# Optimization experiments

Measured on AMD Instinct MI355X. Metric: run time of the kernel, lower is better.

The kernel has to match this reference:

```python
import jax, jax.numpy as jnp
import numpy as np

D_MODEL = 96
N_HEAD = 3
HEAD_DIM = D_MODEL // N_HEAD  # 32
D_FF = 2048
WIDTH = 65
HALF_W = (WIDTH - 1) // 2  # 32
EPS = 1e-5


def layer_norm(x, g, b):
    mu = jnp.mean(x, axis=-1, keepdims=True)
    var = jnp.mean(jnp.square(x - mu), axis=-1, keepdims=True)
    return (x - mu) * jax.lax.rsqrt(var + EPS) * g + b


def setup_inputs() -> dict:
    key = jax.random.key(0)
    ks = jax.random.split(key, 8)
    B, T = 8, 2048
    s = 0.05
    return {
        "x": jax.random.normal(ks[0], (B, D_MODEL, T), dtype=jnp.float32),
        "w_qkv": jax.random.normal(ks[1], (3 * D_MODEL, D_MODEL), dtype=jnp.float32) * s,
        "b_qkv": jnp.zeros((3 * D_MODEL,), dtype=jnp.float32),
        "w_out": jax.random.normal(ks[2], (D_MODEL, D_MODEL), dtype=jnp.float32) * s,
        "b_out": jnp.zeros((D_MODEL,), dtype=jnp.float32),
        "ln1_g": jnp.ones((D_MODEL,), dtype=jnp.float32),
        "ln1_b": jnp.zeros((D_MODEL,), dtype=jnp.float32),
        "w_ff1": jax.random.normal(ks[3], (D_FF, D_MODEL), dtype=jnp.float32) * s,
        "b_ff1": jnp.zeros((D_FF,), dtype=jnp.float32),
        "w_ff2": jax.random.normal(ks[4], (D_MODEL, D_FF), dtype=jnp.float32) * s,
        "b_ff2": jnp.zeros((D_MODEL,), dtype=jnp.float32),
        "ln2_g": jnp.ones((D_MODEL,), dtype=jnp.float32),
        "ln2_b": jnp.zeros((D_MODEL,), dtype=jnp.float32),
        "lnf_g": jnp.ones((D_MODEL,), dtype=jnp.float32),
        "lnf_b": jnp.zeros((D_MODEL,), dtype=jnp.float32),
    }


def reference(x, w_qkv, b_qkv, w_out, b_out, ln1_g, ln1_b, w_ff1, b_ff1,
              w_ff2, b_ff2, ln2_g, ln2_b, lnf_g, lnf_b):
    # x: (B, C, T) -> (B, T, C)
    h = jnp.transpose(x, (0, 2, 1))
    B, T, C = h.shape

    # --- multi-head self-attention with banded mask ---
    qkv = h @ w_qkv.T + b_qkv                      # (B, T, 3C)
    q, k, v = jnp.split(qkv, 3, axis=-1)
    q = q.reshape(B, T, N_HEAD, HEAD_DIM)
    k = k.reshape(B, T, N_HEAD, HEAD_DIM)
    v = v.reshape(B, T, N_HEAD, HEAD_DIM)

    scale = 1.0 / jnp.sqrt(jnp.float32(HEAD_DIM))
    scores = jnp.einsum("bthd,bshd->bhts", q, k) * scale  # (B, H, T, T)

    idx = jnp.arange(T)
    band = jnp.abs(idx[:, None] - idx[None, :]) <= HALF_W  # |i-j| <= half width
    scores = jnp.where(band[None, None], scores, jnp.float32(-jnp.inf))

    attn = jax.nn.softmax(scores, axis=-1)
    ctx = jnp.einsum("bhts,bshd->bthd", attn, v).reshape(B, T, C)
    attn_out = ctx @ w_out.T + b_out

    # --- post-norm encoder layer (dropout inactive / eval mode) ---
    h = layer_norm(h + attn_out, ln1_g, ln1_b)
    ff = jax.nn.relu(h @ w_ff1.T + b_ff1) @ w_ff2.T + b_ff2
    h = layer_norm(h + ff, ln2_g, ln2_b)

    # extra layernorm applied when width is not None
    h = layer_norm(h, lnf_g, lnf_b)

    # (B, T, C) -> (B, C, T)
    return jnp.transpose(h, (0, 2, 1))
```

## Files before the change

kernel.cpp:

```cpp
#include <hip/hip_runtime.h>
#include <hip/hip_bf16.h>

#define B 8
#define T 2048
#define C 96
#define NH 3
#define HD 32
#define FFD 2048
#define HALF_W 32
#define BT (B*T)

typedef __hip_bfloat16 bf16;
typedef __attribute__((ext_vector_type(8))) short short8;
typedef __attribute__((ext_vector_type(4))) short short4v;
typedef __attribute__((ext_vector_type(16))) float floatx16;

__device__ __forceinline__ short f2bs(float v){
    __hip_bfloat16 h = __float2bfloat16(v);
    return *reinterpret_cast<short*>(&h);
}
__device__ __forceinline__ float bs2f(short s){
    unsigned u = ((unsigned)(unsigned short)s) << 16;
    return __uint_as_float(u);
}
__device__ __forceinline__ int imin(int a, int b){ return a < b ? a : b; }
__device__ __forceinline__ int imax(int a, int b){ return a > b ? a : b; }
__device__ __forceinline__ short8 ld_b64x2(const short* p){
    short4v a = *(const short4v*)p;
    short4v b = *(const short4v*)(p + 4);
    short8 v;
    v[0]=a[0]; v[1]=a[1]; v[2]=a[2]; v[3]=a[3];
    v[4]=b[0]; v[5]=b[1]; v[6]=b[2]; v[7]=b[3];
    return v;
}

__global__ void cvtw_kernel(const float* __restrict__ wq, const float* __restrict__ wo,
                            const float* __restrict__ w1, const float* __restrict__ w2,
                            bf16* __restrict__ dst){
    int i = blockIdx.x*256 + threadIdx.x;
    if(i < 27648){
        int e = i&7, lane = (i>>3)&63, r = i>>9;
        int ks = r%6, ot = r/6;
        int o = ot*32 + (lane&31);
        int k = ks*16 + (lane>>5)*8 + e;
        dst[i] = __float2bfloat16(wq[o*96 + k]);
    } else if(i < 36864){
        int j = i - 27648;
        int e = j&7, lane = (j>>3)&63, r = j>>9;
        int ks = r%6, ct = r/6;
        int c = ct*32 + (lane&31);
        int k = ks*16 + (lane>>5)*8 + e;
        dst[i] = __float2bfloat16(wo[c*96 + k]);
    } else if(i < 233472){
        int j = i - 36864;
        int e = j&7, lane = (j>>3)&63, r = j>>9;
        int ks = r%6; r /= 6;
        int w = r%4, jt = r/4;
        int row = jt*128 + w*32 + (lane&31);
        int k = ks*16 + (lane>>5)*8 + e;
        dst[i] = __float2bfloat16(w1[row*96 + k]);
    } else if(i < 430080){
        int j = i - 233472;
        int e = j&7, lane = (j>>3)&63, r = j>>9;
        int ct = r%3; r /= 3;
        int g = r%2; r /= 2;
        int w = r%4, jt = r/4;
        int c = ct*32 + (lane&31);
        int k = jt*128 + w*32 + g*16 + (lane>>5)*8 + e;
        dst[i] = __float2bfloat16(w2[c*FFD + k]);
    }
}

__global__ __launch_bounds__(256) void qkv_kernel(
    const float* __restrict__ x, const bf16* __restrict__ wqs,
    const float* __restrict__ bias, bf16* __restrict__ qswz,
    bf16* __restrict__ kswz, bf16* __restrict__ vbuf){
    __shared__ float xs[96*36];
    int b  = blockIdx.x >> 6;
    int tt = blockIdx.x & 63;
    int t0 = tt * 32;
    for(int e = threadIdx.x; e < 96*8; e += 256){
        int c = e >> 3, t4 = e & 7;
        *(float4*)(xs + c*36 + t4*4) =
            *(const float4*)(x + (size_t)b*C*T + (size_t)c*T + t0 + t4*4);
    }
    __syncthreads();
    const int w = threadIdx.x >> 6, lane = threadIdx.x & 63;
    const int lm = lane & 31, hq = lane >> 5;
    short8 bfr[6];
    #pragma unroll
    for(int ks = 0; ks < 6; ++ks){
        short8 v;
        #pragma unroll
        for(int i = 0; i < 8; ++i)
            v[i] = f2bs(xs[(ks*16 + hq*8 + i)*36 + lm]);
        bfr[ks] = v;
    }
    int nacc = (w == 0) ? 3 : 2;
    int ots[3] = {w, w+4, 8};
    floatx16 acc[3];
    #pragma unroll
    for(int i = 0; i < 3; ++i)
        #pragma unroll
        for(int r = 0; r < 16; ++r) acc[i][r] = 0.f;
    #pragma unroll
    for(int i = 0; i < 3; ++i){
        if(i < nacc){
            #pragma unroll
            for(int ks = 0; ks < 6; ++ks){
                short8 af = *(const short8*)((const short*)wqs
                              + (size_t)(ots[i]*6 + ks)*512 + lane*8);
                acc[i] = __builtin_amdgcn_mfma_f32_32x32x16_bf16(af, bfr[ks], acc[i], 0,0,0);
            }
        }
    }
    #pragma unroll
    for(int i = 0; i < 3; ++i){
        if(i < nacc){
            int ot = ots[i];
            int pkq[4][2];
            #pragma unroll
            for(int q = 0; q < 4; ++q){
                float4 bv = *(const float4*)(bias + ot*32 + 8*q + 4*hq);
                short4v t;
                t[0] = f2bs(acc[i][4*q+0] + bv.x);
                t[1] = f2bs(acc[i][4*q+1] + bv.y);
                t[2] = f2bs(acc[i][4*q+2] + bv.z);
                t[3] = f2bs(acc[i][4*q+3] + bv.w);
                int2 u = *(int2*)&t;
                pkq[q][0] = u.x; pkq[q][1] = u.y;
            }
            if(ot < 6){
                int type = ot/3, hh = ot%3;
                short* base = (short*)(type == 0 ? qswz : kswz)
                            + ((size_t)(b*NH + hh)*64 + tt)*1024 + lane*8;
                #pragma unroll
                for(int g = 0; g < 2; ++g){
                    int a0 = pkq[2*g][0],   a1 = pkq[2*g][1];
                    int b0 = pkq[2*g+1][0], b1v = pkq[2*g+1][1];
                    int ra0 = __shfl_xor(a0, 32),  ra1 = __shfl_xor(a1, 32);
                    int rb0 = __shfl_xor(b0, 32),  rb1 = __shfl_xor(b1v, 32);
                    int4 sfi;
                    sfi.x = hq ? rb0 : a0;
                    sfi.y = hq ? rb1 : a1;
                    sfi.z = hq ? b0  : ra0;
                    sfi.w = hq ? b1v : ra1;
                    *(int4*)(base + g*512) = sfi;
                }
            } else {
                int hh = ot - 6;
                short* rowp = (short*)vbuf + ((size_t)(b*NH + hh)*T + t0 + lm)*32;
                #pragma unroll
                for(int q = 0; q < 4; ++q){
                    int2 u; u.x = pkq[q][0]; u.y = pkq[q][1];
                    *(int2*)(rowp + 8*q + 4*hq) = u;
                }
            }
        }
    }
}

__global__ __launch_bounds__(192) void attn_op_kernel(
    const bf16* __restrict__ qswz, const bf16* __restrict__ kswz,
    const bf16* __restrict__ vbuf, const bf16* __restrict__ wos,
    const float* __restrict__ bias, const float* __restrict__ x,
    const float* __restrict__ g1, const float* __restrict__ bb1,
    bf16* __restrict__ h1b){
    __shared__ __align__(16) short VtS[3*3200];
    __shared__ __align__(16) short PtS[3][3200];
    __shared__ float LsS[3][32];
    __shared__ __align__(16) short ctxS[32*100];
    __shared__ float red1[2][3][32];
    const int tid = threadIdx.x;
    const int w = tid / 64, lane = tid & 63;
    const int lm = lane & 31, hq = lane >> 5;
    int b  = blockIdx.x >> 6;
    int tt = blockIdx.x & 63;
    int t0 = tt * 32;

    short8 wof[6];
    #pragma unroll
    for(int ks = 0; ks < 6; ++ks)
        wof[ks] = *(const short8*)((const short*)wos + (size_t)(w*6 + ks)*512 + lane*8);

    for(int e = tid; e < 576; e += 192){
        int hh = e / 192, rem = e % 192;
        int kp = rem >> 2, d8 = rem & 3;
        const short* vb = (const short*)vbuf + (size_t)(b*NH + hh)*T*32;
        int sa = imin(imax(t0 - 32 + 2*kp, 0), T-1);
        int sb = imin(imax(t0 - 32 + 2*kp + 1, 0), T-1);
        short8 va = *(const short8*)(vb + (size_t)sa*32 + d8*8);
        short8 v2 = *(const short8*)(vb + (size_t)sb*32 + d8*8);
        #pragma unroll
        for(int j = 0; j < 8; ++j){
            int val = (int)(unsigned short)va[j] | ((int)(unsigned short)v2[j] << 16);
            *(int*)(VtS + hh*3200 + (d8*8 + j)*100 + 2*kp) = val;
        }
    }
    const short* qsw = (const short*)qswz + ((size_t)(b*NH + w)*64 + tt)*1024 + lane*8;
    short8 qf0 = *(const short8*)(qsw);
    short8 qf1 = *(const short8*)(qsw + 512);
    floatx16 S[3];
    #pragma unroll
    for(int sub = 0; sub < 3; ++sub){
        int kt = imin(imax(tt - 1 + sub, 0), 63);
        const short* ksw = (const short*)kswz + ((size_t)(b*NH + w)*64 + kt)*1024 + lane*8;
        short8 kf0 = *(const short8*)(ksw);
        short8 kf1 = *(const short8*)(ksw + 512);
        floatx16 z;
        #pragma unroll
        for(int r = 0; r < 16; ++r) z[r] = 0.f;
        z = __builtin_amdgcn_mfma_f32_32x32x16_bf16(kf0, qf0, z, 0,0,0);
        z = __builtin_amdgcn_mfma_f32_32x32x16_bf16(kf1, qf1, z, 0,0,0);
        S[sub] = z;
    }
    const float scale = 0.17677669529663687f;
    float part = 0.f;
    #pragma unroll
    for(int sub = 0; sub < 3; ++sub){
        #pragma unroll
        for(int r = 0; r < 16; ++r){
            int key_local = sub*32 + (r&3) + 8*(r>>2) + 4*hq;
            int s_glob = t0 - 32 + key_local;
            int rel = key_local - lm;
            bool ok = (rel >= 0) && (rel <= 64) && (s_glob >= 0) && (s_glob < T);
            float p = ok ? __expf(S[sub][r]*scale) : 0.f;
            S[sub][r] = p;
            part += p;
        }
    }
    float ltot = part + __shfl_xor(part, 32);
    if(hq == 0) LsS[w][lm] = ltot;
    #pragma unroll
    for(int sub = 0; sub < 3; ++sub){
        #pragma unroll
        for(int q4 = 0; q4 < 4; ++q4){
            int kbase = sub*32 + 8*q4 + 4*hq;
            short4v pk;
            pk[0] = f2bs(S[sub][4*q4+0]);
            pk[1] = f2bs(S[sub][4*q4+1]);
            pk[2] = f2bs(S[sub][4*q4+2]);
            pk[3] = f2bs(S[sub][4*q4+3]);
            *(short4v*)(PtS[w] + lm*100 + kbase) = pk;
        }
    }
    __syncthreads();
    floatx16 O;
    #pragma unroll
    for(int r = 0; r < 16; ++r) O[r] = 0.f;
    #pragma unroll
    for(int ks = 0; ks < 6; ++ks){
        short8 pa = ld_b64x2(PtS[w] + lm*100 + ks*16 + hq*8);
        short8 vf = ld_b64x2(VtS + w*3200 + lm*100 + ks*16 + hq*8);
        O = __builtin_amdgcn_mfma_f32_32x32x16_bf16(pa, vf, O, 0,0,0);
    }
    #pragma unroll
    for(int r = 0; r < 16; ++r){
        int qr = (r&3) + 8*(r>>2) + 4*hq;
        float linv = 1.f / LsS[w][qr];
        ctxS[qr*100 + w*32 + lm] = f2bs(O[r]*linv);
    }
    __syncthreads();

    short8 bfr[6];
    #pragma unroll
    for(int ks = 0; ks < 6; ++ks)
        bfr[ks] = ld_b64x2(ctxS + lm*100 + ks*16 + hq*8);
    floatx16 acc;
    #pragma unroll
    for(int r = 0; r < 16; ++r) acc[r] = 0.f;
    #pragma unroll
    for(int ks = 0; ks < 6; ++ks)
        acc = __builtin_amdgcn_mfma_f32_32x32x16_bf16(wof[ks], bfr[ks], acc, 0,0,0);
    float vals[16];
    float p1 = 0.f, p2 = 0.f;
    #pragma unroll
    for(int q = 0; q < 4; ++q){
        int c = w*32 + 8*q + 4*hq;
        float4 bv = *(const float4*)(bias + c);
        float bva[4] = {bv.x, bv.y, bv.z, bv.w};
        #pragma unroll
        for(int r = 0; r < 4; ++r){
            float xv = x[(size_t)b*C*T + (size_t)(c + r)*T + t0 + lm];
            float v = acc[4*q+r] + bva[r] + xv;
            vals[4*q+r] = v;
            p1 += v; p2 += v*v;
        }
    }
    p1 += __shfl_xor(p1, 32);
    p2 += __shfl_xor(p2, 32);
    if(hq == 0){ red1[0][w][lm] = p1; red1[1][w][lm] = p2; }
    __syncthreads();
    float s  = red1[0][0][lm] + red1[0][1][lm] + red1[0][2][lm];
    float s2 = red1[1][0][lm] + red1[1][1][lm] + red1[1][2][lm];
    float mu = s * (1.0f/96.0f);
    float rstd = rsqrtf(s2*(1.0f/96.0f) - mu*mu + 1e-5f);
    int row = b*T + t0 + lm;
    #pragma unroll
    for(int q = 0; q < 4; ++q){
        int c = w*32 + 8*q + 4*hq;
        float4 gv = *(const float4*)(g1 + c);
        float4 bv = *(const float4*)(bb1 + c);
        float ga[4] = {gv.x, gv.y, gv.z, gv.w};
        float ba[4] = {bv.x, bv.y, bv.z, bv.w};
        short4v pk;
        #pragma unroll
        for(int r = 0; r < 4; ++r)
            pk[r] = f2bs((vals[4*q+r] - mu)*rstd*ga[r] + ba[r]);
        *(short4v*)((short*)h1b + (size_t)row*96 + c) = pk;
    }
}

__global__ __launch_bounds__(256, 1) void ff_ln_kernel(
    const bf16* __restrict__ h1b,
    const bf16* __restrict__ w1s, const float* __restrict__ b1,
    const bf16* __restrict__ w2s, const float* __restrict__ b2,
    const float* __restrict__ g2, const float* __restrict__ bt2,
    const float* __restrict__ gf, const float* __restrict__ btf,
    float* __restrict__ out){
    __shared__ float redp[4*2*3*1088];
    __shared__ float zt[96*65];
    const int tid = threadIdx.x;
    const int w4 = tid >> 6, lane = tid & 63;
    const int lm = lane & 31, hq = lane >> 5;
    const int r0 = blockIdx.x * 64;
    short8 hf[2][6];
    #pragma unroll
    for(int mt = 0; mt < 2; ++mt)
        #pragma unroll
        for(int ks = 0; ks < 6; ++ks)
            hf[mt][ks] = *(const short8*)((const short*)h1b
                       + (size_t)(r0 + mt*32 + lm)*96 + ks*16 + hq*8);
    floatx16 acc2[2][3];
    #pragma unroll
    for(int mt = 0; mt < 2; ++mt)
        #pragma unroll
        for(int i = 0; i < 3; ++i)
            #pragma unroll
            for(int r = 0; r < 16; ++r) acc2[mt][i][r] = 0.f;

    const short* w1p = (const short*)w1s + (size_t)w4*6*512 + lane*8;
    const short* w2p = (const short*)w2s + (size_t)w4*2*3*512 + lane*8;
    short8 cw1[6], cw2[6];
    #pragma unroll
    for(int ks = 0; ks < 6; ++ks)
        cw1[ks] = *(const short8*)(w1p + ks*512);
    #pragma unroll
    for(int g = 0; g < 2; ++g)
        #pragma unroll
        for(int ct = 0; ct < 3; ++ct)
            cw2[g*3 + ct] = *(const short8*)(w2p + ((size_t)g*3 + ct)*512);

    #pragma unroll
    for(int jt = 0; jt < 16; ++jt){
        const int jn = (jt + 1) & 15;
        short8 nw1[6], nw2[6];
        #pragma unroll
        for(int ks = 0; ks < 6; ++ks)
            nw1[ks] = *(const short8*)(w1p + (size_t)jn*4*6*512 + ks*512);
        #pragma unroll
        for(int g = 0; g < 2; ++g)
            #pragma unroll
            for(int ct = 0; ct < 3; ++ct)
                nw2[g*3 + ct] = *(const short8*)(w2p + ((size_t)jn*4*2*3 + g*3 + ct)*512);
        floatx16 a0, a1;
        #pragma unroll
        for(int r = 0; r < 16; ++r){ a0[r] = 0.f; a1[r] = 0.f; }
        #pragma unroll
        for(int ks = 0; ks < 6; ++ks){
            a0 = __builtin_amdgcn_mfma_f32_32x32x16_bf16(cw1[ks], hf[0][ks], a0, 0,0,0);
            a1 = __builtin_amdgcn_mfma_f32_32x32x16_bf16(cw1[ks], hf[1][ks], a1, 0,0,0);
        }
        int pk[2][4][2];
        #pragma unroll
        for(int q = 0; q < 4; ++q){
            float4 bv = *(const float4*)(b1 + jt*128 + w4*32 + 8*q + 4*hq);
            float bva[4] = {bv.x, bv.y, bv.z, bv.w};
            short4v t0v, t1v;
            #pragma unroll
            for(int r = 0; r < 4; ++r){
                float v0 = a0[4*q+r] + bva[r];
                float v1 = a1[4*q+r] + bva[r];
                t0v[r] = f2bs(v0 > 0.f ? v0 : 0.f);
                t1v[r] = f2bs(v1 > 0.f ? v1 : 0.f);
            }
            int2 u0 = *(int2*)&t0v; int2 u1 = *(int2*)&t1v;
            pk[0][q][0] = u0.x; pk[0][q][1] = u0.y;
            pk[1][q][0] = u1.x; pk[1][q][1] = u1.y;
        }
        #pragma unroll
        for(int g = 0; g < 2; ++g){
            short8 sf[2];
            #pragma unroll
            for(int mt = 0; mt < 2; ++mt){
                int a0i = pk[mt][2*g][0],   a1i = pk[mt][2*g][1];
                int b0i = pk[mt][2*g+1][0], b1i = pk[mt][2*g+1][1];
                int ra0 = __shfl_xor(a0i, 32), ra1 = __shfl_xor(a1i, 32);
                int rb0 = __shfl_xor(b0i, 32), rb1 = __shfl_xor(b1i, 32);
                int4 sfi;
                sfi.x = hq ? rb0 : a0i;
                sfi.y = hq ? rb1 : a1i;
                sfi.z = hq ? b0i : ra0;
                sfi.w = hq ? b1i : ra1;
                sf[mt] = *(short8*)&sfi;
            }
            #pragma unroll
            for(int ct = 0; ct < 3; ++ct){
                acc2[0][ct] = __builtin_amdgcn_mfma_f32_32x32x16_bf16(cw2[g*3+ct], sf[0], acc2[0][ct], 0,0,0);
                acc2[1][ct] = __builtin_amdgcn_mfma_f32_32x32x16_bf16(cw2[g*3+ct], sf[1], acc2[1][ct], 0,0,0);
            }
        }
        #pragma unroll
        for(int ks = 0; ks < 6; ++ks) cw1[ks] = nw1[ks];
        #pragma unroll
        for(int i = 0; i < 6; ++i) cw2[i] = nw2[i];
    }
    __syncthreads();
    #pragma unroll
    for(int mt = 0; mt < 2; ++mt)
        #pragma unroll
        for(int ct = 0; ct < 3; ++ct)
            #pragma unroll
            for(int q = 0; q < 4; ++q)
                #pragma unroll
                for(int r = 0; r < 4; ++r)
                    redp[((w4*2 + mt)*3 + ct)*1088 + lane*17 + 4*q + r] = acc2[mt][ct][4*q+r];
    __syncthreads();
    if(w4 < 2){
        const int mt = w4;
        const int rr = r0 + mt*32;
        float vals[48];
        float p1 = 0.f, p2 = 0.f;
        #pragma unroll
        for(int ct = 0; ct < 3; ++ct){
            #pragma unroll
            for(int q = 0; q < 4; ++q){
                int c = ct*32 + 8*q + 4*hq;
                float4 bv = *(const float4*)(b2 + c);
                short4v hv = *(const short4v*)((const short*)h1b + (size_t)(rr + lm)*96 + c);
                float bva[4] = {bv.x, bv.y, bv.z, bv.w};
                #pragma unroll
                for(int r = 0; r < 4; ++r){
                    float v = redp[((0*2 + mt)*3 + ct)*1088 + lane*17 + 4*q + r]
                            + redp[((1*2 + mt)*3 + ct)*1088 + lane*17 + 4*q + r]
                            + redp[((2*2 + mt)*3 + ct)*1088 + lane*17 + 4*q + r]
                            + redp[((3*2 + mt)*3 + ct)*1088 + lane*17 + 4*q + r]
                            + bva[r] + bs2f(hv[r]);
                    vals[ct*16 + 4*q + r] = v;
                    p1 += v; p2 += v*v;
                }
            }
        }
        p1 += __shfl_xor(p1, 32);
        p2 += __shfl_xor(p2, 32);
        float mu = p1*(1.0f/96.0f);
        float rstd = rsqrtf(p2*(1.0f/96.0f) - mu*mu + 1e-5f);
        float q1 = 0.f, q2 = 0.f;
        #pragma unroll
        for(int ct = 0; ct < 3; ++ct){
            #pragma unroll
            for(int q = 0; q < 4; ++q){
                int c = ct*32 + 8*q + 4*hq;
                float4 gv = *(const float4*)(g2 + c);
                float4 bv = *(const float4*)(bt2 + c);
                float ga[4] = {gv.x, gv.y, gv.z, gv.w};
                float ba[4] = {bv.x, bv.y, bv.z, bv.w};
                #pragma unroll
                for(int r = 0; r < 4; ++r){
                    float y = (vals[ct*16+4*q+r] - mu)*rstd*ga[r] + ba[r];
                    vals[ct*16+4*q+r] = y;
                    q1 += y; q2 += y*y;
                }
            }
        }
        q1 += __shfl_xor(q1, 32);
        q2 += __shfl_xor(q2, 32);
        float mu2 = q1*(1.0f/96.0f);
        float rstd2 = rsqrtf(q2*(1.0f/96.0f) - mu2*mu2 + 1e-5f);
        #pragma unroll
        for(int ct = 0; ct < 3; ++ct){
            #pragma unroll
            for(int q = 0; q < 4; ++q){
                int c = ct*32 + 8*q + 4*hq;
                float4 gv = *(const float4*)(gf + c);
                float4 bv = *(const float4*)(btf + c);
                float ga[4] = {gv.x, gv.y, gv.z, gv.w};
                float ba[4] = {bv.x, bv.y, bv.z, bv.w};
                #pragma unroll
                for(int r = 0; r < 4; ++r)
                    zt[(c + r)*65 + mt*32 + lm] = (vals[ct*16+4*q+r] - mu2)*rstd2*ga[r] + ba[r];
            }
        }
    }
    __syncthreads();
    int bb  = r0 / T;
    int t0g = r0 % T;
    for(int e = tid; e < 96*64; e += 256){
        int c = e >> 6, tt = e & 63;
        out[(size_t)bb*C*T + (size_t)c*T + t0g + tt] = zt[c*65 + tt];
    }
}

extern "C" void kernel_launch(void* const* d_in, const int* in_sizes, int n_in,
                              void* d_out, int out_size, void* d_ws, size_t ws_size,
                              hipStream_t stream) {
    const float* x     = (const float*)d_in[0];
    const float* w_qkv = (const float*)d_in[1];
    const float* b_qkv = (const float*)d_in[2];
    const float* w_out = (const float*)d_in[3];
    const float* b_out = (const float*)d_in[4];
    const float* ln1_g = (const float*)d_in[5];
    const float* ln1_b = (const float*)d_in[6];
    const float* w_ff1 = (const float*)d_in[7];
    const float* b_ff1 = (const float*)d_in[8];
    const float* w_ff2 = (const float*)d_in[9];
    const float* b_ff2 = (const float*)d_in[10];
    const float* ln2_g = (const float*)d_in[11];
    const float* ln2_b = (const float*)d_in[12];
    const float* lnf_g = (const float*)d_in[13];
    const float* lnf_b = (const float*)d_in[14];
    float* out = (float*)d_out;

    char* wsb = (char*)d_ws;
    bf16*  qswz  = (bf16*)wsb;
    bf16*  kswz  = (bf16*)(wsb + 3145728);
    bf16*  vbuf  = (bf16*)(wsb + 6291456);
    bf16*  h1b   = (bf16*)(wsb + 9437184);
    bf16*  wts   = (bf16*)(wsb + 12582912);
    bf16*  wqs   = wts;
    bf16*  wos   = wts + 27648;
    bf16*  w1s   = wts + 36864;
    bf16*  w2s   = wts + 233472;

    cvtw_kernel   <<<1680, 256, 0, stream>>>(w_qkv, w_out, w_ff1, w_ff2, wts);
    qkv_kernel    <<<BT/32, 256, 0, stream>>>(x, wqs, b_qkv, qswz, kswz, vbuf);
    attn_op_kernel<<<B*(T/32), 192, 0, stream>>>(qswz, kswz, vbuf, wos, b_out, x,
                                                 ln1_g, ln1_b, h1b);
    ff_ln_kernel  <<<BT/64, 256, 0, stream>>>(h1b, w1s, b_ff1, w2s, b_ff2,
                                              ln2_g, ln2_b, lnf_g, lnf_b, out);
}
```

Baseline: 126.6 us.

## Fuse QKV, banded attention, out-proj and FFN into one encoder kernel

Merges the QKV projection, attention with output projection and LN1, and the FFN with both layernorms into a single kernel. Each block handles 32 tokens and recomputes K and V for a 96-token halo instead of reading them back from global memory. This removes the q/k/v and h1 intermediate round-trips through global memory and two kernel launches. In exchange it repeats the K/V projection work about three times and runs the FFN with 32-row tiles and 192 threads instead of 64-row tiles, which means less weight reuse per block.

```diff
diff --git a/kernel.cpp b/kernel.cpp
--- a/kernel.cpp
+++ b/kernel.cpp
@@ -23,8 +23,6 @@
     unsigned u = ((unsigned)(unsigned short)s) << 16;
     return __uint_as_float(u);
 }
-__device__ __forceinline__ int imin(int a, int b){ return a < b ? a : b; }
-__device__ __forceinline__ int imax(int a, int b){ return a > b ? a : b; }
 __device__ __forceinline__ short8 ld_b64x2(const short* p){
     short4v a = *(const short4v*)p;
     short4v b = *(const short4v*)(p + 4);
@@ -32,6 +30,31 @@
     v[0]=a[0]; v[1]=a[1]; v[2]=a[2]; v[3]=a[3];
     v[4]=b[0]; v[5]=b[1]; v[6]=b[2]; v[7]=b[3];
     return v;
+}
+__device__ __forceinline__ int4 exch_pair(int a0,int a1,int b0,int b1,int hq){
+    int ra0=__shfl_xor(a0,32), ra1=__shfl_xor(a1,32);
+    int rb0=__shfl_xor(b0,32), rb1=__shfl_xor(b1,32);
+    int4 s;
+    s.x = hq ? rb0 : a0;
+    s.y = hq ? rb1 : a1;
+    s.z = hq ? b0  : ra0;
+    s.w = hq ? b1  : ra1;
+    return s;
+}
+__device__ __forceinline__ void proj_pack(const floatx16& acc, const float* bias32, int hq,
+                                          short8& f0, short8& f1){
+    int pkq[4][2];
+    #pragma unroll
+    for(int q = 0; q < 4; ++q){
+        float4 bv = *(const float4*)(bias32 + 8*q + 4*hq);
+        short4v t;
+        t[0]=f2bs(acc[4*q+0]+bv.x); t[1]=f2bs(acc[4*q+1]+bv.y);
+        t[2]=f2bs(acc[4*q+2]+bv.z); t[3]=f2bs(acc[4*q+3]+bv.w);
+        int2 u = *(int2*)&t; pkq[q][0]=u.x; pkq[q][1]=u.y;
+    }
+    int4 r0 = exch_pair(pkq[0][0],pkq[0][1],pkq[1][0],pkq[1][1],hq);
+    int4 r1 = exch_pair(pkq[2][0],pkq[2][1],pkq[3][0],pkq[3][1],hq);
+    f0 = *(short8*)&r0; f1 = *(short8*)&r1;
 }
 
 __global__ void cvtw_kernel(const float* __restrict__ wq, const float* __restrict__ wo,
@@ -71,147 +94,115 @@
     }
 }
 
-__global__ __launch_bounds__(256) void qkv_kernel(
-    const float* __restrict__ x, const bf16* __restrict__ wqs,
-    const float* __restrict__ bias, bf16* __restrict__ qswz,
-    bf16* __restrict__ kswz, bf16* __restrict__ vbuf){
-    __shared__ float xs[96*36];
-    int b  = blockIdx.x >> 6;
-    int tt = blockIdx.x & 63;
-    int t0 = tt * 32;
-    for(int e = threadIdx.x; e < 96*8; e += 256){
-        int c = e >> 3, t4 = e & 7;
-        *(float4*)(xs + c*36 + t4*4) =
-            *(const float4*)(x + (size_t)b*C*T + (size_t)c*T + t0 + t4*4);
-    }
-    __syncthreads();
-    const int w = threadIdx.x >> 6, lane = threadIdx.x & 63;
-    const int lm = lane & 31, hq = lane >> 5;
-    short8 bfr[6];
-    #pragma unroll
-    for(int ks = 0; ks < 6; ++ks){
-        short8 v;
-        #pragma unroll
-        for(int i = 0; i < 8; ++i)
-            v[i] = f2bs(xs[(ks*16 + hq*8 + i)*36 + lm]);
-        bfr[ks] = v;
-    }
-    int nacc = (w == 0) ? 3 : 2;
-    int ots[3] = {w, w+4, 8};
-    floatx16 acc[3];
-    #pragma unroll
-    for(int i = 0; i < 3; ++i)
-        #pragma unroll
-        for(int r = 0; r < 16; ++r) acc[i][r] = 0.f;
-    #pragma unroll
-    for(int i = 0; i < 3; ++i){
-        if(i < nacc){
-            #pragma unroll
-            for(int ks = 0; ks < 6; ++ks){
-                short8 af = *(const short8*)((const short*)wqs
-                              + (size_t)(ots[i]*6 + ks)*512 + lane*8);
-                acc[i] = __builtin_amdgcn_mfma_f32_32x32x16_bf16(af, bfr[ks], acc[i], 0,0,0);
-            }
-        }
-    }
-    #pragma unroll
-    for(int i = 0; i < 3; ++i){
-        if(i < nacc){
-            int ot = ots[i];
-            int pkq[4][2];
-            #pragma unroll
-            for(int q = 0; q < 4; ++q){
-                float4 bv = *(const float4*)(bias + ot*32 + 8*q + 4*hq);
-                short4v t;
-                t[0] = f2bs(acc[i][4*q+0] + bv.x);
-                t[1] = f2bs(acc[i][4*q+1] + bv.y);
-                t[2] = f2bs(acc[i][4*q+2] + bv.z);
-                t[3] = f2bs(acc[i][4*q+3] + bv.w);
-                int2 u = *(int2*)&t;
-                pkq[q][0] = u.x; pkq[q][1] = u.y;
-            }
-            if(ot < 6){
-                int type = ot/3, hh = ot%3;
-                short* base = (short*)(type == 0 ? qswz : kswz)
-                            + ((size_t)(b*NH + hh)*64 + tt)*1024 + lane*8;
-                #pragma unroll
-                for(int g = 0; g < 2; ++g){
-                    int a0 = pkq[2*g][0],   a1 = pkq[2*g][1];
-                    int b0 = pkq[2*g+1][0], b1v = pkq[2*g+1][1];
-                    int ra0 = __shfl_xor(a0, 32),  ra1 = __shfl_xor(a1, 32);
-                    int rb0 = __shfl_xor(b0, 32),  rb1 = __shfl_xor(b1v, 32);
-                    int4 sfi;
-                    sfi.x = hq ? rb0 : a0;
-                    sfi.y = hq ? rb1 : a1;
-                    sfi.z = hq ? b0  : ra0;
-                    sfi.w = hq ? b1v : ra1;
-                    *(int4*)(base + g*512) = sfi;
-                }
-            } else {
-                int hh = ot - 6;
-                short* rowp = (short*)vbuf + ((size_t)(b*NH + hh)*T + t0 + lm)*32;
-                #pragma unroll
-                for(int q = 0; q < 4; ++q){
-                    int2 u; u.x = pkq[q][0]; u.y = pkq[q][1];
-                    *(int2*)(rowp + 8*q + 4*hq) = u;
-                }
-            }
-        }
-    }
-}
-
-__global__ __launch_bounds__(192) void attn_op_kernel(
-    const bf16* __restrict__ qswz, const bf16* __restrict__ kswz,
-    const bf16* __restrict__ vbuf, const bf16* __restrict__ wos,
-    const float* __restrict__ bias, const float* __restrict__ x,
+__global__ __launch_bounds__(192, 2) void encoder_kernel(
+    const float* __restrict__ x,
+    const bf16* __restrict__ wqs, const bf16* __restrict__ wos,
+    const bf16* __restrict__ w1s, const bf16* __restrict__ w2s,
+    const float* __restrict__ b_qkv, const float* __restrict__ b_out,
     const float* __restrict__ g1, const float* __restrict__ bb1,
-    bf16* __restrict__ h1b){
-    __shared__ __align__(16) short VtS[3*3200];
-    __shared__ __align__(16) short PtS[3][3200];
-    __shared__ float LsS[3][32];
-    __shared__ __align__(16) short ctxS[32*100];
-    __shared__ float red1[2][3][32];
+    const float* __restrict__ b1, const float* __restrict__ b2,
+    const float* __restrict__ g2, const float* __restrict__ bt2,
+    const float* __restrict__ gf, const float* __restrict__ btf,
+    float* __restrict__ out){
+    __shared__ __align__(16) char smem[73088];
+    float* XS   = (float*)smem;
+    short* PTS  = (short*)smem;
+    float* REDP = (float*)smem;
+    short* VTS  = (short*)(smem + 39936);
+    float* ZT   = (float*)(smem + 39936);
+    short* CTX  = (short*)(smem + 59136);
+    short* H1S  = (short*)(smem + 65536);
+    float* LSS  = (float*)(smem + 71936);
+    float* RED1 = (float*)(smem + 72320);
+
     const int tid = threadIdx.x;
     const int w = tid / 64, lane = tid & 63;
     const int lm = lane & 31, hq = lane >> 5;
-    int b  = blockIdx.x >> 6;
-    int tt = blockIdx.x & 63;
-    int t0 = tt * 32;
+    const int b  = blockIdx.x >> 6;
+    const int tt = blockIdx.x & 63;
+    const int t0 = tt * 32;
+    const float* xb = x + (size_t)b*C*T;
 
     short8 wof[6];
     #pragma unroll
     for(int ks = 0; ks < 6; ++ks)
         wof[ks] = *(const short8*)((const short*)wos + (size_t)(w*6 + ks)*512 + lane*8);
 
-    for(int e = tid; e < 576; e += 192){
-        int hh = e / 192, rem = e % 192;
-        int kp = rem >> 2, d8 = rem & 3;
-        const short* vb = (const short*)vbuf + (size_t)(b*NH + hh)*T*32;
-        int sa = imin(imax(t0 - 32 + 2*kp, 0), T-1);
-        int sb = imin(imax(t0 - 32 + 2*kp + 1, 0), T-1);
-        short8 va = *(const short8*)(vb + (size_t)sa*32 + d8*8);
-        short8 v2 = *(const short8*)(vb + (size_t)sb*32 + d8*8);
-        #pragma unroll
-        for(int j = 0; j < 8; ++j){
-            int val = (int)(unsigned short)va[j] | ((int)(unsigned short)v2[j] << 16);
-            *(int*)(VtS + hh*3200 + (d8*8 + j)*100 + 2*kp) = val;
-        }
-    }
-    const short* qsw = (const short*)qswz + ((size_t)(b*NH + w)*64 + tt)*1024 + lane*8;
-    short8 qf0 = *(const short8*)(qsw);
-    short8 qf1 = *(const short8*)(qsw + 512);
+    int tg0 = t0 - 32;
+    if(tg0 >= 0 && t0 + 64 <= T){
+        for(int e = tid; e < 96*24; e += 192){
+            int c = e / 24, q4 = e % 24;
+            *(float4*)(XS + c*104 + q4*4) = *(const float4*)(xb + (size_t)c*T + tg0 + q4*4);
+        }
+    } else {
+        for(int e = tid; e < 96*96; e += 192){
+            int c = e / 96, j = e % 96;
+            int t = tg0 + j; t = t < 0 ? 0 : (t > T-1 ? T-1 : t);
+            XS[c*104 + j] = xb[(size_t)c*T + t];
+        }
+    }
+    __syncthreads();
+
+    short8 kwf[6], vwf[6];
+    #pragma unroll
+    for(int ks = 0; ks < 6; ++ks){
+        kwf[ks] = *(const short8*)((const short*)wqs + (size_t)((3+w)*6 + ks)*512 + lane*8);
+        vwf[ks] = *(const short8*)((const short*)wqs + (size_t)((6+w)*6 + ks)*512 + lane*8);
+    }
+    short8 kf[3][2]; short8 qf0, qf1;
+    #pragma unroll
+    for(int tau = 0; tau < 3; ++tau){
+        short8 bfr[6];
+        #pragma unroll
+        for(int ks = 0; ks < 6; ++ks){
+            short8 vv;
+            #pragma unroll
+            for(int i = 0; i < 8; ++i)
+                vv[i] = f2bs(XS[(ks*16 + hq*8 + i)*104 + tau*32 + lm]);
+            bfr[ks] = vv;
+        }
+        floatx16 acc;
+        #pragma unroll
+        for(int r = 0; r < 16; ++r) acc[r] = 0.f;
+        #pragma unroll
+        for(int ks = 0; ks < 6; ++ks)
+            acc = __builtin_amdgcn_mfma_f32_32x32x16_bf16(kwf[ks], bfr[ks], acc, 0,0,0);
+        proj_pack(acc, b_qkv + (3+w)*32, hq, kf[tau][0], kf[tau][1]);
+        #pragma unroll
+        for(int r = 0; r < 16; ++r) acc[r] = 0.f;
+        #pragma unroll
+        for(int ks = 0; ks < 6; ++ks)
+            acc = __builtin_amdgcn_mfma_f32_32x32x16_bf16(vwf[ks], bfr[ks], acc, 0,0,0);
+        #pragma unroll
+        for(int q = 0; q < 4; ++q){
+            float4 bv = *(const float4*)(b_qkv + (6+w)*32 + 8*q + 4*hq);
+            float bva[4] = {bv.x, bv.y, bv.z, bv.w};
+            #pragma unroll
+            for(int r = 0; r < 4; ++r)
+                VTS[w*3200 + (8*q + 4*hq + r)*100 + tau*32 + lm] = f2bs(acc[4*q+r] + bva[r]);
+        }
+        if(tau == 1){
+            floatx16 qa;
+            #pragma unroll
+            for(int r = 0; r < 16; ++r) qa[r] = 0.f;
+            #pragma unroll
+            for(int ks = 0; ks < 6; ++ks){
+                short8 qwf = *(const short8*)((const short*)wqs + (size_t)(w*6 + ks)*512 + lane*8);
+                qa = __builtin_amdgcn_mfma_f32_32x32x16_bf16(qwf, bfr[ks], qa, 0,0,0);
+            }
+            proj_pack(qa, b_qkv + w*32, hq, qf0, qf1);
+        }
+    }
+    __syncthreads();
+
     floatx16 S[3];
     #pragma unroll
     for(int sub = 0; sub < 3; ++sub){
-        int kt = imin(imax(tt - 1 + sub, 0), 63);
-        const short* ksw = (const short*)kswz + ((size_t)(b*NH + w)*64 + kt)*1024 + lane*8;
-        short8 kf0 = *(const short8*)(ksw);
-        short8 kf1 = *(const short8*)(ksw + 512);
         floatx16 z;
         #pragma unroll
         for(int r = 0; r < 16; ++r) z[r] = 0.f;
-        z = __builtin_amdgcn_mfma_f32_32x32x16_bf16(kf0, qf0, z, 0,0,0);
-        z = __builtin_amdgcn_mfma_f32_32x32x16_bf16(kf1, qf1, z, 0,0,0);
+        z = __builtin_amdgcn_mfma_f32_32x32x16_bf16(kf[sub][0], qf0, z, 0,0,0);
+        z = __builtin_amdgcn_mfma_f32_32x32x16_bf16(kf[sub][1], qf1, z, 0,0,0);
         S[sub] = z;
     }
     const float scale = 0.17677669529663687f;
@@ -230,274 +221,228 @@
         }
     }
     float ltot = part + __shfl_xor(part, 32);
-    if(hq == 0) LsS[w][lm] = ltot;
+    if(hq == 0) LSS[w*32 + lm] = ltot;
     #pragma unroll
     for(int sub = 0; sub < 3; ++sub){
         #pragma unroll
         for(int q4 = 0; q4 < 4; ++q4){
             int kbase = sub*32 + 8*q4 + 4*hq;
-            short4v pk;
-            pk[0] = f2bs(S[sub][4*q4+0]);
-            pk[1] = f2bs(S[sub][4*q4+1]);
-            pk[2] = f2bs(S[sub][4*q4+2]);
-            pk[3] = f2bs(S[sub][4*q4+3]);
-            *(short4v*)(PtS[w] + lm*100 + kbase) = pk;
-        }
-    }
-    __syncthreads();
+            short4v pk4;
+            pk4[0] = f2bs(S[sub][4*q4+0]);
+            pk4[1] = f2bs(S[sub][4*q4+1]);
+            pk4[2] = f2bs(S[sub][4*q4+2]);
+            pk4[3] = f2bs(S[sub][4*q4+3]);
+            *(short4v*)(PTS + w*3200 + lm*100 + kbase) = pk4;
+        }
+    }
     floatx16 O;
     #pragma unroll
     for(int r = 0; r < 16; ++r) O[r] = 0.f;
     #pragma unroll
     for(int ks = 0; ks < 6; ++ks){
-        short8 pa = ld_b64x2(PtS[w] + lm*100 + ks*16 + hq*8);
-        short8 vf = ld_b64x2(VtS + w*3200 + lm*100 + ks*16 + hq*8);
+        short8 pa = ld_b64x2(PTS + w*3200 + lm*100 + ks*16 + hq*8);
+        short8 vf = ld_b64x2(VTS + w*3200 + lm*100 + ks*16 + hq*8);
         O = __builtin_amdgcn_mfma_f32_32x32x16_bf16(pa, vf, O, 0,0,0);
     }
     #pragma unroll
     for(int r = 0; r < 16; ++r){
         int qr = (r&3) + 8*(r>>2) + 4*hq;
-        float linv = 1.f / LsS[w][qr];
-        ctxS[qr*100 + w*32 + lm] = f2bs(O[r]*linv);
-    }
-    __syncthreads();
-
-    short8 bfr[6];
+        float linv = 1.f / LSS[w*32 + qr];
+        CTX[qr*100 + w*32 + lm] = f2bs(O[r]*linv);
+    }
+    __syncthreads();
+
+    short8 cbfr[6];
     #pragma unroll
     for(int ks = 0; ks < 6; ++ks)
-        bfr[ks] = ld_b64x2(ctxS + lm*100 + ks*16 + hq*8);
-    floatx16 acc;
-    #pragma unroll
-    for(int r = 0; r < 16; ++r) acc[r] = 0.f;
+        cbfr[ks] = ld_b64x2(CTX + lm*100 + ks*16 + hq*8);
+    floatx16 pacc;
+    #pragma unroll
+    for(int r = 0; r < 16; ++r) pacc[r] = 0.f;
     #pragma unroll
     for(int ks = 0; ks < 6; ++ks)
-        acc = __builtin_amdgcn_mfma_f32_32x32x16_bf16(wof[ks], bfr[ks], acc, 0,0,0);
+        pacc = __builtin_amdgcn_mfma_f32_32x32x16_bf16(wof[ks], cbfr[ks], pacc, 0,0,0);
     float vals[16];
     float p1 = 0.f, p2 = 0.f;
     #pragma unroll
     for(int q = 0; q < 4; ++q){
         int c = w*32 + 8*q + 4*hq;
-        float4 bv = *(const float4*)(bias + c);
+        float4 bv = *(const float4*)(b_out + c);
         float bva[4] = {bv.x, bv.y, bv.z, bv.w};
         #pragma unroll
         for(int r = 0; r < 4; ++r){
-            float xv = x[(size_t)b*C*T + (size_t)(c + r)*T + t0 + lm];
-            float v = acc[4*q+r] + bva[r] + xv;
+            float xv = xb[(size_t)(c + r)*T + t0 + lm];
+            float v = pacc[4*q+r] + bva[r] + xv;
             vals[4*q+r] = v;
             p1 += v; p2 += v*v;
         }
     }
     p1 += __shfl_xor(p1, 32);
     p2 += __shfl_xor(p2, 32);
-    if(hq == 0){ red1[0][w][lm] = p1; red1[1][w][lm] = p2; }
-    __syncthreads();
-    float s  = red1[0][0][lm] + red1[0][1][lm] + red1[0][2][lm];
-    float s2 = red1[1][0][lm] + red1[1][1][lm] + red1[1][2][lm];
-    float mu = s * (1.0f/96.0f);
-    float rstd = rsqrtf(s2*(1.0f/96.0f) - mu*mu + 1e-5f);
-    int row = b*T + t0 + lm;
+    if(hq == 0){ RED1[w*32 + lm] = p1; RED1[96 + w*32 + lm] = p2; }
+    __syncthreads();
+    {
+        float s  = RED1[lm] + RED1[32 + lm] + RED1[64 + lm];
+        float s2 = RED1[96 + lm] + RED1[128 + lm] + RED1[160 + lm];
+        float mu = s * (1.0f/96.0f);
+        float rstd = rsqrtf(s2*(1.0f/96.0f) - mu*mu + 1e-5f);
+        #pragma unroll
+        for(int q = 0; q < 4; ++q){
+            int c = w*32 + 8*q + 4*hq;
+            float4 gv = *(const float4*)(g1 + c);
+            float4 bv = *(const float4*)(bb1 + c);
+            float ga[4] = {gv.x, gv.y, gv.z, gv.w};
+            float ba[4] = {bv.x, bv.y, bv.z, bv.w};
+            short4v pkv;
+            #pragma unroll
+            for(int r = 0; r < 4; ++r)
+                pkv[r] = f2bs((vals[4*q+r] - mu)*rstd*ga[r] + ba[r]);
+            *(short4v*)(H1S + lm*100 + c) = pkv;
+        }
+    }
+    __syncthreads();
+
+    short8 hf[6];
+    #pragma unroll
+    for(int ks = 0; ks < 6; ++ks)
+        hf[ks] = ld_b64x2(H1S + lm*100 + ks*16 + hq*8);
+    floatx16 acc2[3];
+    #pragma unroll
+    for(int i = 0; i < 3; ++i)
+        #pragma unroll
+        for(int r = 0; r < 16; ++r) acc2[i][r] = 0.f;
+    const short* w1b = (const short*)w1s + lane*8;
+    const short* w2b = (const short*)w2s + lane*8;
+    short8 cw1[6], cw2[6];
+    #pragma unroll
+    for(int ks = 0; ks < 6; ++ks)
+        cw1[ks] = *(const short8*)(w1b + (size_t)(w*6 + ks)*512);
+    #pragma unroll
+    for(int g = 0; g < 2; ++g)
+        #pragma unroll
+        for(int ct = 0; ct < 3; ++ct)
+            cw2[g*3 + ct] = *(const short8*)(w2b + (size_t)((w*2 + g)*3 + ct)*512);
+    for(int J = w; J < 64; J += 3){
+        int Jn = (J + 3 < 64) ? J + 3 : w;
+        short8 nw1[6], nw2[6];
+        #pragma unroll
+        for(int ks = 0; ks < 6; ++ks)
+            nw1[ks] = *(const short8*)(w1b + (size_t)(Jn*6 + ks)*512);
+        #pragma unroll
+        for(int g = 0; g < 2; ++g)
+            #pragma unroll
+            for(int ct = 0; ct < 3; ++ct)
+                nw2[g*3 + ct] = *(const short8*)(w2b + (size_t)((Jn*2 + g)*3 + ct)*512);
+        floatx16 a0;
+        #pragma unroll
+        for(int r = 0; r < 16; ++r) a0[r] = 0.f;
+        #pragma unroll
+        for(int ks = 0; ks < 6; ++ks)
+            a0 = __builtin_amdgcn_mfma_f32_32x32x16_bf16(cw1[ks], hf[ks], a0, 0,0,0);
+        int pk[4][2];
+        #pragma unroll
+        for(int q = 0; q < 4; ++q){
+            float4 bv = *(const float4*)(b1 + J*32 + 8*q + 4*hq);
+            float bva[4] = {bv.x, bv.y, bv.z, bv.w};
+            short4v tv;
+            #pragma unroll
+            for(int r = 0; r < 4; ++r){
+                float v0 = a0[4*q+r] + bva[r];
+                tv[r] = f2bs(v0 > 0.f ? v0 : 0.f);
+            }
+            int2 u = *(int2*)&tv; pk[q][0] = u.x; pk[q][1] = u.y;
+        }
+        #pragma unroll
+        for(int g = 0; g < 2; ++g){
+            int4 sfi = exch_pair(pk[2*g][0], pk[2*g][1], pk[2*g+1][0], pk[2*g+1][1], hq);
+            short8 sf = *(short8*)&sfi;
+            #pragma unroll
+            for(int ct = 0; ct < 3; ++ct)
+                acc2[ct] = __builtin_amdgcn_mfma_f32_32x32x16_bf16(cw2[g*3+ct], sf, acc2[ct], 0,0,0);
+        }
+        #pragma unroll
+        for(int ks = 0; ks < 6; ++ks) cw1[ks] = nw1[ks];
+        #pragma unroll
+        for(int i = 0; i < 6; ++i) cw2[i] = nw2[i];
+    }
+    #pragma unroll
+    for(int ct = 0; ct < 3; ++ct)
+        #pragma unroll
+        for(int q = 0; q < 4; ++q)
+            #pragma unroll
+            for(int r = 0; r < 4; ++r)
+                REDP[(w*3 + ct)*1088 + lane*17 + 4*q + r] = acc2[ct][4*q+r];
+    __syncthreads();
+
+    float fv[16];
+    float e1 = 0.f, e2 = 0.f;
     #pragma unroll
     for(int q = 0; q < 4; ++q){
         int c = w*32 + 8*q + 4*hq;
-        float4 gv = *(const float4*)(g1 + c);
-        float4 bv = *(const float4*)(bb1 + c);
-        float ga[4] = {gv.x, gv.y, gv.z, gv.w};
-        float ba[4] = {bv.x, bv.y, bv.z, bv.w};
-        short4v pk;
-        #pragma unroll
-        for(int r = 0; r < 4; ++r)
-            pk[r] = f2bs((vals[4*q+r] - mu)*rstd*ga[r] + ba[r]);
-        *(short4v*)((short*)h1b + (size_t)row*96 + c) = pk;
-    }
-}
-
-__global__ __launch_bounds__(256, 1) void ff_ln_kernel(
-    const bf16* __restrict__ h1b,
-    const bf16* __restrict__ w1s, const float* __restrict__ b1,
-    const bf16* __restrict__ w2s, const float* __restrict__ b2,
-    const float* __restrict__ g2, const float* __restrict__ bt2,
-    const float* __restrict__ gf, const float* __restrict__ btf,
-    float* __restrict__ out){
-    __shared__ float redp[4*2*3*1088];
-    __shared__ float zt[96*65];
-    const int tid = threadIdx.x;
-    const int w4 = tid >> 6, lane = tid & 63;
-    const int lm = lane & 31, hq = lane >> 5;
-    const int r0 = blockIdx.x * 64;
-    short8 hf[2][6];
-    #pragma unroll
-    for(int mt = 0; mt < 2; ++mt)
-        #pragma unroll
-        for(int ks = 0; ks < 6; ++ks)
-            hf[mt][ks] = *(const short8*)((const short*)h1b
-                       + (size_t)(r0 + mt*32 + lm)*96 + ks*16 + hq*8);
-    floatx16 acc2[2][3];
-    #pragma unroll
-    for(int mt = 0; mt < 2; ++mt)
-        #pragma unroll
-        for(int i = 0; i < 3; ++i)
-            #pragma unroll
-            for(int r = 0; r < 16; ++r) acc2[mt][i][r] = 0.f;
-
-    const short* w1p = (const short*)w1s + (size_t)w4*6*512 + lane*8;
-    const short* w2p = (const short*)w2s + (size_t)w4*2*3*512 + lane*8;
-    short8 cw1[6], cw2[6];
-    #pragma unroll
-    for(int ks = 0; ks < 6; ++ks)
-        cw1[ks] = *(const short8*)(w1p + ks*512);
-    #pragma unroll
-    for(int g = 0; g < 2; ++g)
-        #pragma unroll
-        for(int ct = 0; ct < 3; ++ct)
-            cw2[g*3 + ct] = *(const short8*)(w2p + ((size_t)g*3 + ct)*512);
-
-    #pragma unroll
-    for(int jt = 0; jt < 16; ++jt){
-        const int jn = (jt + 1) & 15;
-        short8 nw1[6], nw2[6];
-        #pragma unroll
-        for(int ks = 0; ks < 6; ++ks)
-            nw1[ks] = *(const short8*)(w1p + (size_t)jn*4*6*512 + ks*512);
-        #pragma unroll
-        for(int g = 0; g < 2; ++g)
-            #pragma unroll
-            for(int ct = 0; ct < 3; ++ct)
-                nw2[g*3 + ct] = *(const short8*)(w2p + ((size_t)jn*4*2*3 + g*3 + ct)*512);
-        floatx16 a0, a1;
-        #pragma unroll
-        for(int r = 0; r < 16; ++r){ a0[r] = 0.f; a1[r] = 0.f; }
-        #pragma unroll
-        for(int ks = 0; ks < 6; ++ks){
-            a0 = __builtin_amdgcn_mfma_f32_32x32x16_bf16(cw1[ks], hf[0][ks], a0, 0,0,0);
-            a1 = __builtin_amdgcn_mfma_f32_32x32x16_bf16(cw1[ks], hf[1][ks], a1, 0,0,0);
-        }
-        int pk[2][4][2];
+        float4 bv = *(const float4*)(b2 + c);
+        float bva[4] = {bv.x, bv.y, bv.z, bv.w};
+        #pragma unroll
+        for(int r = 0; r < 4; ++r){
+            float v = REDP[(0 + w)*1088 + lane*17 + 4*q + r]
+                    + REDP[(3 + w)*1088 + lane*17 + 4*q + r]
+                    + REDP[(6 + w)*1088 + lane*17 + 4*q + r]
+                    + bva[r] + bs2f(H1S[lm*100 + c + r]);
+            fv[4*q+r] = v;
+            e1 += v; e2 += v*v;
+        }
+    }
+    e1 += __shfl_xor(e1, 32);
+    e2 += __shfl_xor(e2, 32);
+    if(hq == 0){ RED1[w*32 + lm] = e1; RED1[96 + w*32 + lm] = e2; }
+    __syncthreads();
+    float f1 = 0.f, f2 = 0.f;
+    {
+        float s  = RED1[lm] + RED1[32 + lm] + RED1[64 + lm];
+        float s2 = RED1[96 + lm] + RED1[128 + lm] + RED1[160 + lm];
+        float mu = s * (1.0f/96.0f);
+        float rstd = rsqrtf(s2*(1.0f/96.0f) - mu*mu + 1e-5f);
         #pragma unroll
         for(int q = 0; q < 4; ++q){
-            float4 bv = *(const float4*)(b1 + jt*128 + w4*32 + 8*q + 4*hq);
-            float bva[4] = {bv.x, bv.y, bv.z, bv.w};
-            short4v t0v, t1v;
+            int c = w*32 + 8*q + 4*hq;
+            float4 gv = *(const float4*)(g2 + c);
+            float4 bv = *(const float4*)(bt2 + c);
+            float ga[4] = {gv.x, gv.y, gv.z, gv.w};
+            float ba[4] = {bv.x, bv.y, bv.z, bv.w};
             #pragma unroll
             for(int r = 0; r < 4; ++r){
-                float v0 = a0[4*q+r] + bva[r];
-                float v1 = a1[4*q+r] + bva[r];
-                t0v[r] = f2bs(v0 > 0.f ? v0 : 0.f);
-                t1v[r] = f2bs(v1 > 0.f ? v1 : 0.f);
+                float y = (fv[4*q+r] - mu)*rstd*ga[r] + ba[r];
+                fv[4*q+r] = y;
+                f1 += y; f2 += y*y;
             }
-            int2 u0 = *(int2*)&t0v; int2 u1 = *(int2*)&t1v;
-            pk[0][q][0] = u0.x; pk[0][q][1] = u0.y;
-            pk[1][q][0] = u1.x; pk[1][q][1] = u1.y;
-        }
-        #pragma unroll
-        for(int g = 0; g < 2; ++g){
-            short8 sf[2];
-            #pragma unroll
-            for(int mt = 0; mt < 2; ++mt){
-                int a0i = pk[mt][2*g][0],   a1i = pk[mt][2*g][1];
-                int b0i = pk[mt][2*g+1][0], b1i = pk[mt][2*g+1][1];
-                int ra0 = __shfl_xor(a0i, 32), ra1 = __shfl_xor(a1i, 32);
-                int rb0 = __shfl_xor(b0i, 32), rb1 = __shfl_xor(b1i, 32);
-                int4 sfi;
-                sfi.x = hq ? rb0 : a0i;
-                sfi.y = hq ? rb1 : a1i;
-                sfi.z = hq ? b0i : ra0;
-                sfi.w = hq ? b1i : ra1;
-                sf[mt] = *(short8*)&sfi;
-            }
-            #pragma unroll
-            for(int ct = 0; ct < 3; ++ct){
-                acc2[0][ct] = __builtin_amdgcn_mfma_f32_32x32x16_bf16(cw2[g*3+ct], sf[0], acc2[0][ct], 0,0,0);
-                acc2[1][ct] = __builtin_amdgcn_mfma_f32_32x32x16_bf16(cw2[g*3+ct], sf[1], acc2[1][ct], 0,0,0);
-            }
-        }
-        #pragma unroll
-        for(int ks = 0; ks < 6; ++ks) cw1[ks] = nw1[ks];
-        #pragma unroll
-        for(int i = 0; i < 6; ++i) cw2[i] = nw2[i];
-    }
-    __syncthreads();
-    #pragma unroll
-    for(int mt = 0; mt < 2; ++mt)
-        #pragma unroll
-        for(int ct = 0; ct < 3; ++ct)
-            #pragma unroll
-            for(int q = 0; q < 4; ++q)
-                #pragma unroll
-                for(int r = 0; r < 4; ++r)
-                    redp[((w4*2 + mt)*3 + ct)*1088 + lane*17 + 4*q + r] = acc2[mt][ct][4*q+r];
-    __syncthreads();
-    if(w4 < 2){
-        const int mt = w4;
-        const int rr = r0 + mt*32;
-        float vals[48];
-        float p1 = 0.f, p2 = 0.f;
-        #pragma unroll
-        for(int ct = 0; ct < 3; ++ct){
-            #pragma unroll
-            for(int q = 0; q < 4; ++q){
-                int c = ct*32 + 8*q + 4*hq;
-                float4 bv = *(const float4*)(b2 + c);
-                short4v hv = *(const short4v*)((const short*)h1b + (size_t)(rr + lm)*96 + c);
-                float bva[4] = {bv.x, bv.y, bv.z, bv.w};
-                #pragma unroll
-                for(int r = 0; r < 4; ++r){
-                    float v = redp[((0*2 + mt)*3 + ct)*1088 + lane*17 + 4*q + r]
-                            + redp[((1*2 + mt)*3 + ct)*1088 + lane*17 + 4*q + r]
-                            + redp[((2*2 + mt)*3 + ct)*1088 + lane*17 + 4*q + r]
-                            + redp[((3*2 + mt)*3 + ct)*1088 + lane*17 + 4*q + r]
-                            + bva[r] + bs2f(hv[r]);
-                    vals[ct*16 + 4*q + r] = v;
-                    p1 += v; p2 += v*v;
-                }
-            }
-        }
-        p1 += __shfl_xor(p1, 32);
-        p2 += __shfl_xor(p2, 32);
-        float mu = p1*(1.0f/96.0f);
-        float rstd = rsqrtf(p2*(1.0f/96.0f) - mu*mu + 1e-5f);
-        float q1 = 0.f, q2 = 0.f;
-        #pragma unroll
-        for(int ct = 0; ct < 3; ++ct){
-            #pragma unroll
-            for(int q = 0; q < 4; ++q){
-                int c = ct*32 + 8*q + 4*hq;
-                float4 gv = *(const float4*)(g2 + c);
-                float4 bv = *(const float4*)(bt2 + c);
-                float ga[4] = {gv.x, gv.y, gv.z, gv.w};
-                float ba[4] = {bv.x, bv.y, bv.z, bv.w};
-                #pragma unroll
-                for(int r = 0; r < 4; ++r){
-                    float y = (vals[ct*16+4*q+r] - mu)*rstd*ga[r] + ba[r];
-                    vals[ct*16+4*q+r] = y;
-                    q1 += y; q2 += y*y;
-                }
-            }
-        }
-        q1 += __shfl_xor(q1, 32);
-        q2 += __shfl_xor(q2, 32);
-        float mu2 = q1*(1.0f/96.0f);
-        float rstd2 = rsqrtf(q2*(1.0f/96.0f) - mu2*mu2 + 1e-5f);
-        #pragma unroll
-        for(int ct = 0; ct < 3; ++ct){
-            #pragma unroll
-            for(int q = 0; q < 4; ++q){
-                int c = ct*32 + 8*q + 4*hq;
-                float4 gv = *(const float4*)(gf + c);
-                float4 bv = *(const float4*)(btf + c);
-                float ga[4] = {gv.x, gv.y, gv.z, gv.w};
-                float ba[4] = {bv.x, bv.y, bv.z, bv.w};
-                #pragma unroll
-                for(int r = 0; r < 4; ++r)
-                    zt[(c + r)*65 + mt*32 + lm] = (vals[ct*16+4*q+r] - mu2)*rstd2*ga[r] + ba[r];
-            }
-        }
-    }
-    __syncthreads();
-    int bb  = r0 / T;
-    int t0g = r0 % T;
-    for(int e = tid; e < 96*64; e += 256){
-        int c = e >> 6, tt = e & 63;
-        out[(size_t)bb*C*T + (size_t)c*T + t0g + tt] = zt[c*65 + tt];
+        }
+    }
+    f1 += __shfl_xor(f1, 32);
+    f2 += __shfl_xor(f2, 32);
+    __syncthreads();
+    if(hq == 0){ RED1[w*32 + lm] = f1; RED1[96 + w*32 + lm] = f2; }
+    __syncthreads();
+    {
+        float s  = RED1[lm] + RED1[32 + lm] + RED1[64 + lm];
+        float s2 = RED1[96 + lm] + RED1[128 + lm] + RED1[160 + lm];
+        float mu = s * (1.0f/96.0f);
+        float rstd = rsqrtf(s2*(1.0f/96.0f) - mu*mu + 1e-5f);
+        #pragma unroll
+        for(int q = 0; q < 4; ++q){
+            int c = w*32 + 8*q + 4*hq;
+            float4 gv = *(const float4*)(gf + c);
+            float4 bv = *(const float4*)(btf + c);
+            float ga[4] = {gv.x, gv.y, gv.z, gv.w};
+            float ba[4] = {bv.x, bv.y, bv.z, bv.w};
+            #pragma unroll
+            for(int r = 0; r < 4; ++r)
+                ZT[(c + r)*36 + lm] = (fv[4*q+r] - mu)*rstd*ga[r] + ba[r];
+        }
+    }
+    __syncthreads();
+    float* ob = out + (size_t)b*C*T + t0;
+    for(int e = tid; e < 96*8; e += 192){
+        int c = e >> 3, qq = e & 7;
+        *(float4*)(ob + (size_t)c*T + qq*4) = *(const float4*)(ZT + c*36 + qq*4);
     }
 }
 
@@ -521,21 +466,15 @@
     const float* lnf_b = (const float*)d_in[14];
     float* out = (float*)d_out;
 
-    char* wsb = (char*)d_ws;
-    bf16*  qswz  = (bf16*)wsb;
-    bf16*  kswz  = (bf16*)(wsb + 3145728);
-    bf16*  vbuf  = (bf16*)(wsb + 6291456);
-    bf16*  h1b   = (bf16*)(wsb + 9437184);
-    bf16*  wts   = (bf16*)(wsb + 12582912);
-    bf16*  wqs   = wts;
-    bf16*  wos   = wts + 27648;
-    bf16*  w1s   = wts + 36864;
-    bf16*  w2s   = wts + 233472;
+    bf16* wts = (bf16*)d_ws;
+    bf16* wqs = wts;
+    bf16* wos = wts + 27648;
+    bf16* w1s = wts + 36864;
+    bf16* w2s = wts + 233472;
 
     cvtw_kernel   <<<1680, 256, 0, stream>>>(w_qkv, w_out, w_ff1, w_ff2, wts);
-    qkv_kernel    <<<BT/32, 256, 0, stream>>>(x, wqs, b_qkv, qswz, kswz, vbuf);
-    attn_op_kernel<<<B*(T/32), 192, 0, stream>>>(qswz, kswz, vbuf, wos, b_out, x,
-                                                 ln1_g, ln1_b, h1b);
-    ff_ln_kernel  <<<BT/64, 256, 0, stream>>>(h1b, w1s, b_ff1, w2s, b_ff2,
-                                              ln2_g, ln2_b, lnf_g, lnf_b, out);
-}
+    encoder_kernel<<<B*(T/32), 192, 0, stream>>>(x, wqs, wos, w1s, w2s,
+                                                 b_qkv, b_out, ln1_g, ln1_b,
+                                                 b_ff1, b_ff2, ln2_g, ln2_b,
+                                                 lnf_g, lnf_b, out);
+}
```

Result: no change. 124.6 us (median of 2 runs) (-1.5%).
